# Kernel optimization log

Measured on AMD Instinct MI355X. Metric: run time of the kernel, lower is better.

Reference implementation:

```python
import jax, jax.numpy as jnp
import numpy as np
from jax.ops import segment_sum

N_NODES = 50000


def gcn_conv(x, W, b, src, dst, n_nodes):
    """Standard PyG GCNConv: self-loops + symmetric deg^-1/2 normalization."""
    h = x @ W  # [N, H]
    loop = jnp.arange(n_nodes, dtype=src.dtype)
    s = jnp.concatenate([src, loop])
    d = jnp.concatenate([dst, loop])
    deg = segment_sum(jnp.ones_like(d, dtype=h.dtype), d, num_segments=n_nodes)
    dinv = jnp.where(deg > 0, jax.lax.rsqrt(deg), 0.0)
    norm = dinv[s] * dinv[d]  # [E+N]
    msg = h[s] * norm[:, None]  # gather + scale
    out = segment_sum(msg, d, num_segments=n_nodes)  # scatter-add
    return out + b


def setup_inputs() -> dict:
    key = jax.random.key(0)
    ks = jax.random.split(key, 12)
    node_in, hidden = 256, 128
    n_edges = 1_600_000
    x = jax.random.normal(ks[0], (N_NODES, node_in), dtype=jnp.float32)
    edge_index = jax.random.randint(ks[1], (2, n_edges), 0, N_NODES, dtype=jnp.int64)

    def glorot(k, fan_in, fan_out):
        lim = np.sqrt(6.0 / (fan_in + fan_out)).astype(np.float32)
        return jax.random.uniform(k, (fan_in, fan_out), jnp.float32, -lim, lim)

    W1 = glorot(ks[2], node_in, hidden)
    b1 = jnp.zeros((hidden,), jnp.float32)
    W2 = glorot(ks[3], hidden, hidden)
    b2 = jnp.zeros((hidden,), jnp.float32)
    W3 = glorot(ks[4], 2 * hidden, hidden)
    b3 = jnp.zeros((hidden,), jnp.float32)
    W4 = glorot(ks[5], hidden, 1)
    b4 = jnp.zeros((1,), jnp.float32)
    return {"x": x, "edge_index": edge_index, "W1": W1, "b1": b1,
            "W2": W2, "b2": b2, "W3": W3, "b3": b3, "W4": W4, "b4": b4}


def reference(x, edge_index, W1, b1, W2, b2, W3, b3, W4, b4):
    src, dst = edge_index[0], edge_index[1]
    h = gcn_conv(x, W1, b1, src, dst, N_NODES)
    h = jax.nn.relu(h)  # dropout is identity in eval mode
    h = gcn_conv(h, W2, b2, src, dst, N_NODES)
    # gather node pairs per edge, concat, MLP edge classifier
    ef = jnp.concatenate([h[src], h[dst]], axis=1)  # [E, 2H]
    z = jax.nn.relu(ef @ W3 + b3)
    scores = jax.nn.sigmoid(z @ W4 + b4)
    return scores.squeeze(-1)
```

## Files before the change

kernel.cpp:

```cpp
#include <hip/hip_runtime.h>
#include <math.h>

typedef unsigned short ushort_t;
typedef __attribute__((ext_vector_type(8))) short bf16x8;
typedef __attribute__((ext_vector_type(4))) float f32x4;

__device__ __forceinline__ float bf2f(unsigned short u) {
    union { unsigned int i; float f; } x; x.i = ((unsigned int)u) << 16; return x.f;
}
__device__ __forceinline__ unsigned short f2bf(float f) {
    union { float f; unsigned int i; } x; x.f = f;
    unsigned int lsb = (x.i >> 16) & 1u;
    return (unsigned short)((x.i + 0x7fffu + lsb) >> 16);
}


__global__ __launch_bounds__(1024) void detect_i64(const int* __restrict__ ei,
                                                   int nwords, int* __restrict__ flag) {
    __shared__ int s_any;
    if (threadIdx.x == 0) s_any = 0;
    __syncthreads();
    int any = 0;
    for (int i = threadIdx.x; 2 * i + 1 < nwords; i += 1024)
        if (ei[2 * i + 1] != 0) any = 1;
    if (any) s_any = 1;
    __syncthreads();
    if (threadIdx.x == 0) flag[0] = (s_any == 0) ? 1 : 0;
}

__global__ __launch_bounds__(256) void normalize_idx(const int* __restrict__ ei, int E,
                                                     const int* __restrict__ flag,
                                                     int* __restrict__ s_out,
                                                     int* __restrict__ d_out) {
    int e = blockIdx.x * 256 + threadIdx.x;
    if (e >= E) return;
    if (flag[0]) {
        s_out[e] = ei[2 * e];
        d_out[e] = ei[2 * (E + e)];
    } else {
        s_out[e] = ei[e];
        d_out[e] = ei[E + e];
    }
}


__global__ __launch_bounds__(256) void zero_i32(int* __restrict__ p, int n) {
    int i = blockIdx.x * 256 + threadIdx.x;
    if (i < n) p[i] = 0;
}

__global__ __launch_bounds__(256) void count_deg_part(const int* __restrict__ dst,
                                                      int* __restrict__ deg,
                                                      int E, int RB) {
    int xcd = blockIdx.x & 7;
    int e = (blockIdx.x >> 3) * 256 + threadIdx.x;
    if (e >= E) return;
    int d = dst[e];
    if ((unsigned)(d - xcd * RB) < (unsigned)RB) atomicAdd(&deg[d], 1);
}

__global__ __launch_bounds__(1024) void scan_kernel(const int* __restrict__ deg,
                                                    int* __restrict__ offs,
                                                    int* __restrict__ cursor,
                                                    float* __restrict__ dinv, int n) {
    __shared__ int wsum[16];
    __shared__ int s_carry;
    int tid = threadIdx.x, lane = tid & 63, wid = tid >> 6;
    if (tid == 0) s_carry = 0;
    __syncthreads();
    for (int base = 0; base < n; base += 1024) {
        int i = base + tid;
        int v = (i < n) ? deg[i] : 0;
        int x = v;
        #pragma unroll
        for (int d = 1; d < 64; d <<= 1) {
            int y = __shfl_up(x, d, 64);
            if (lane >= d) x += y;
        }
        if (lane == 63) wsum[wid] = x;
        __syncthreads();
        int carry = s_carry;
        __syncthreads();
        if (tid == 0) {
            int run = 0;
            #pragma unroll
            for (int w = 0; w < 16; ++w) { int t = wsum[w]; wsum[w] = run; run += t; }
            s_carry = carry + run;
        }
        __syncthreads();
        if (i < n) {
            int excl = carry + wsum[wid] + (x - v);
            offs[i] = excl;
            cursor[i] = excl;
            dinv[i] = rsqrtf((float)(v + 1));
        }
        __syncthreads();
    }
    if (tid == 0) offs[n] = s_carry;
}

__global__ __launch_bounds__(256) void fill_csr_part(const int* __restrict__ src,
                                                     const int* __restrict__ dst,
                                                     int* __restrict__ cursor,
                                                     int2* __restrict__ csr_se,
                                                     int E, int RB) {
    int xcd = blockIdx.x & 7;
    int e = (blockIdx.x >> 3) * 256 + threadIdx.x;
    if (e >= E) return;
    int d = dst[e];
    if ((unsigned)(d - xcd * RB) < (unsigned)RB) {
        int pos = atomicAdd(&cursor[d], 1);
        csr_se[pos] = make_int2(src[e], e);
    }
}

__global__ __launch_bounds__(256) void fill_seg(const int* __restrict__ offs,
                                                int* __restrict__ csr_dst, int n_nodes) {
    int wid = threadIdx.x >> 6, lane = threadIdx.x & 63;
    int node = blockIdx.x * 4 + wid;
    if (node >= n_nodes) return;
    int beg = offs[node], end = offs[node + 1];
    for (int i = beg + lane; i < end; i += 64) csr_dst[i] = node;
}


__global__ __launch_bounds__(256) void conv_weights(const float* __restrict__ W1,
                                                    const float* __restrict__ W2,
                                                    const float* __restrict__ W3,
                                                    ushort_t* __restrict__ Wt1,
                                                    ushort_t* __restrict__ Wt2,
                                                    ushort_t* __restrict__ Wt3a,
                                                    ushort_t* __restrict__ Wt3b) {
    int t = blockIdx.x * 256 + threadIdx.x;
    if (t < 32768) {
        int k = t >> 7, n = t & 127;
        Wt1[n * 256 + k] = f2bf(W1[t]);
    } else if (t < 49152) {
        int u = t - 32768; int k = u >> 7, n = u & 127;
        Wt2[n * 128 + k] = f2bf(W2[u]);
    } else if (t < 65536) {
        int u = t - 49152; int k = u >> 7, n = u & 127;
        Wt3a[n * 128 + k] = f2bf(W3[u]);
    } else if (t < 81920) {
        int u = t - 65536; int k = u >> 7, n = u & 127;
        Wt3b[n * 128 + k] = f2bf(W3[128 * 128 + u]);
    }
}


#define ASTR 40
#define BSTR 136

__global__ __launch_bounds__(256) void gemm_mfma(const float* __restrict__ A,
                                                 const ushort_t* __restrict__ Wt,
                                                 void* __restrict__ outv,
                                                 const float* __restrict__ dinv,
                                                 const float* __restrict__ bias,
                                                 int M, int K, int out_bf16) {
    __shared__ __attribute__((aligned(16))) ushort_t Bt[128 * BSTR];
    __shared__ __attribute__((aligned(16))) ushort_t As[64 * ASTR];
    int tid = threadIdx.x;
    int wave = tid >> 6, lane = tid & 63;
    int l15 = lane & 15, lg = lane >> 4;
    int block_m = blockIdx.x * 64;
    f32x4 acc[8];
    #pragma unroll
    for (int i = 0; i < 8; ++i) acc[i] = (f32x4){0.f, 0.f, 0.f, 0.f};

    for (int kh = 0; kh < K; kh += 128) {
        #pragma unroll
        for (int i = 0; i < 16; ++i) {
            int u = i * 256 + tid;
            int col = u >> 5;
            int kq = (u & 31) * 4;
            ushort4 w = *(const ushort4*)(&Wt[(size_t)col * K + kh + kq]);
            *(ushort4*)(&Bt[col * BSTR + kq]) = w;
        }
        for (int k0 = kh; k0 < kh + 128; k0 += 32) {
            #pragma unroll
            for (int rep = 0; rep < 2; ++rep) {
                int unit = rep * 256 + tid;
                int r = unit >> 3;
                int kc = (unit & 7) * 4;
                int gr = block_m + r;
                int grc = gr < M ? gr : M - 1;
                float4 v = *(const float4*)(&A[(size_t)grc * K + k0 + kc]);
                if (gr >= M) v = make_float4(0.f, 0.f, 0.f, 0.f);
                ushort4 p;
                p.x = f2bf(v.x); p.y = f2bf(v.y); p.z = f2bf(v.z); p.w = f2bf(v.w);
                *(ushort4*)(&As[r * ASTR + kc]) = p;
            }
            __syncthreads();
            bf16x8 af = *(const bf16x8*)(&As[(wave * 16 + l15) * ASTR + lg * 8]);
            #pragma unroll
            for (int nf = 0; nf < 8; ++nf) {
                bf16x8 bf = *(const bf16x8*)(&Bt[(nf * 16 + l15) * BSTR +
                                                 (k0 - kh) + lg * 8]);
                acc[nf] = __builtin_amdgcn_mfma_f32_16x16x32_bf16(af, bf, acc[nf],
                                                                  0, 0, 0);
            }
            __syncthreads();
        }
    }
    int orow = block_m + wave * 16 + lg * 4;
    #pragma unroll
    for (int nf = 0; nf < 8; ++nf) {
        int col = nf * 16 + l15;
        float bb = bias ? bias[col] : 0.f;
        #pragma unroll
        for (int j = 0; j < 4; ++j) {
            int m = orow + j;
            if (m < M) {
                float s = dinv ? dinv[m] : 1.f;
                float o = acc[nf][j] * s + bb;
                if (out_bf16)
                    ((ushort_t*)outv)[(size_t)m * 128 + col] = f2bf(o);
                else
                    ((float*)outv)[(size_t)m * 128 + col] = o;
            }
        }
    }
}


__global__ __launch_bounds__(256) void pull_agg(const ushort_t* __restrict__ g,
                                                const int2* __restrict__ csr_se,
                                                const int* __restrict__ offs,
                                                const float* __restrict__ dinv,
                                                const float* __restrict__ bias,
                                                float* __restrict__ out,
                                                int n_nodes, int do_relu) {
    int wid = threadIdx.x >> 6;
    int lane = threadIdx.x & 63;
    int node = blockIdx.x * 4 + wid;
    if (node >= n_nodes) return;
    int beg = offs[node], end = offs[node + 1];
    ushort2 sv = *(const ushort2*)(g + (size_t)node * 128 + 2 * lane);
    float a0 = bf2f(sv.x), a1 = bf2f(sv.y);
    int i = beg;
    for (; i + 4 <= end; i += 4) {
        int s0 = csr_se[i].x, s1 = csr_se[i + 1].x;
        int s2 = csr_se[i + 2].x, s3 = csr_se[i + 3].x;
        ushort2 v0 = *(const ushort2*)(g + (size_t)s0 * 128 + 2 * lane);
        ushort2 v1 = *(const ushort2*)(g + (size_t)s1 * 128 + 2 * lane);
        ushort2 v2 = *(const ushort2*)(g + (size_t)s2 * 128 + 2 * lane);
        ushort2 v3 = *(const ushort2*)(g + (size_t)s3 * 128 + 2 * lane);
        a0 += bf2f(v0.x) + bf2f(v1.x) + bf2f(v2.x) + bf2f(v3.x);
        a1 += bf2f(v0.y) + bf2f(v1.y) + bf2f(v2.y) + bf2f(v3.y);
    }
    for (; i < end; ++i) {
        ushort2 v = *(const ushort2*)(g + (size_t)csr_se[i].x * 128 + 2 * lane);
        a0 += bf2f(v.x); a1 += bf2f(v.y);
    }
    float s = dinv[node];
    float v0 = a0 * s + bias[2 * lane];
    float v1 = a1 * s + bias[2 * lane + 1];
    if (do_relu) { v0 = fmaxf(v0, 0.f); v1 = fmaxf(v1, 0.f); }
    *(float2*)(&out[(size_t)node * 128 + 2 * lane]) = make_float2(v0, v1);
}


__global__ __launch_bounds__(256) void edge_score_csr(const ushort_t* __restrict__ u,
                                                      const ushort_t* __restrict__ v,
                                                      const int2* __restrict__ csr_se,
                                                      const int* __restrict__ csr_dst,
                                                      const float* __restrict__ W4,
                                                      const float* __restrict__ b4,
                                                      float* __restrict__ out, int E) {
    __shared__ int2 s_se[32];
    __shared__ int s_dst[32];
    int tid = threadIdx.x;
    long base = (long)blockIdx.x * 32;
    if (tid < 32) {
        long p = base + tid;
        s_se[tid] = (p < E) ? csr_se[p] : make_int2(0, 0);
    } else if (tid < 64) {
        long p = base + (tid - 32);
        s_dst[tid - 32] = (p < E) ? csr_dst[p] : 0;
    }
    __syncthreads();
    int grp = tid >> 5;
    int lane = tid & 31;
    float4 w4 = *(const float4*)(&W4[lane * 4]);
    float b4v = b4[0];
    #pragma unroll
    for (int i = 0; i < 4; ++i) {
        int ei = grp * 4 + i;
        int s = s_se[ei].x, d = s_dst[ei];
        ushort4 a = *(const ushort4*)(u + (size_t)s * 128 + lane * 4);
        ushort4 b = *(const ushort4*)(v + (size_t)d * 128 + lane * 4);
        float p = fmaxf(bf2f(a.x) + bf2f(b.x), 0.f) * w4.x
                + fmaxf(bf2f(a.y) + bf2f(b.y), 0.f) * w4.y
                + fmaxf(bf2f(a.z) + bf2f(b.z), 0.f) * w4.z
                + fmaxf(bf2f(a.w) + bf2f(b.w), 0.f) * w4.w;
        #pragma unroll
        for (int m = 16; m >= 1; m >>= 1) p += __shfl_xor(p, m, 64);
        if (lane == 0 && base + ei < E)
            out[s_se[ei].y] = 1.f / (1.f + expf(-(p + b4v)));
    }
}


extern "C" void kernel_launch(void* const* d_in, const int* in_sizes, int n_in,
                              void* d_out, int out_size, void* d_ws, size_t ws_size,
                              hipStream_t stream) {
    const float* x  = (const float*)d_in[0];
    const int*   ei = (const int*)d_in[1];
    const float* W1 = (const float*)d_in[2];
    const float* b1 = (const float*)d_in[3];
    const float* W2 = (const float*)d_in[4];
    const float* b2 = (const float*)d_in[5];
    const float* W3 = (const float*)d_in[6];
    const float* b3 = (const float*)d_in[7];
    const float* W4 = (const float*)d_in[8];
    const float* b4 = (const float*)d_in[9];

    int N = in_sizes[0] / 256;
    int E = in_sizes[1] / 2;

    char* ws = (char*)d_ws;
    size_t off = 0;
    auto alloc = [&](size_t bytes) -> void* {
        void* p = ws + off;
        off += (bytes + 255) & ~(size_t)255;
        return p;
    };
    int*      flag    = (int*)     alloc(256);
    int*      srcn    = (int*)     alloc((size_t)E * 4);
    int*      dstn    = (int*)     alloc((size_t)E * 4);
    int*      deg     = (int*)     alloc((size_t)N * 4);
    int*      offs    = (int*)     alloc((size_t)(N + 1) * 4);
    int*      cursor  = (int*)     alloc((size_t)N * 4);
    float*    dinv    = (float*)   alloc((size_t)N * 4);
    int2*     csr_se  = (int2*)    alloc((size_t)E * 8);
    int*      csr_dst = (int*)     alloc((size_t)E * 4);
    ushort_t* gbuf    = (ushort_t*)alloc((size_t)N * 128 * 2);
    ushort_t* ubuf    = (ushort_t*)alloc((size_t)N * 128 * 2);
    ushort_t* vbuf    = (ushort_t*)alloc((size_t)N * 128 * 2);
    float*    hbuf    = (float*)   alloc((size_t)N * 128 * 4);
    ushort_t* Wt1     = (ushort_t*)alloc(128 * 256 * 2);
    ushort_t* Wt2     = (ushort_t*)alloc(128 * 128 * 2);
    ushort_t* Wt3a    = (ushort_t*)alloc(128 * 128 * 2);
    ushort_t* Wt3b    = (ushort_t*)alloc(128 * 128 * 2);
    (void)ws_size; (void)n_in; (void)out_size;

    float* outp = (float*)d_out;
    int gE = (E + 255) / 256;
    int gN4 = (N + 3) / 4;
    int RB = (N + 7) / 8;

    int nwords = (2 * E < 4096) ? 2 * E : 4096;
    detect_i64<<<1, 1024, 0, stream>>>(ei, nwords, flag);
    normalize_idx<<<gE, 256, 0, stream>>>(ei, E, flag, srcn, dstn);
    conv_weights<<<320, 256, 0, stream>>>(W1, W2, W3, Wt1, Wt2, Wt3a, Wt3b);

    zero_i32<<<(N + 255) / 256, 256, 0, stream>>>(deg, N);
    count_deg_part<<<gE * 8, 256, 0, stream>>>(dstn, deg, E, RB);
    scan_kernel<<<1, 1024, 0, stream>>>(deg, offs, cursor, dinv, N);
    fill_csr_part<<<gE * 8, 256, 0, stream>>>(srcn, dstn, cursor, csr_se, E, RB);
    fill_seg<<<gN4, 256, 0, stream>>>(offs, csr_dst, N);

    int gM = (N + 63) / 64;
    gemm_mfma<<<gM, 256, 0, stream>>>(x, Wt1, gbuf, dinv, nullptr, N, 256, 1);
    pull_agg<<<gN4, 256, 0, stream>>>(gbuf, csr_se, offs, dinv, b1, hbuf, N, 1);
    gemm_mfma<<<gM, 256, 0, stream>>>(hbuf, Wt2, gbuf, dinv, nullptr, N, 128, 1);
    pull_agg<<<gN4, 256, 0, stream>>>(gbuf, csr_se, offs, dinv, b2, hbuf, N, 0);
    gemm_mfma<<<gM, 256, 0, stream>>>(hbuf, Wt3a, ubuf, nullptr, nullptr, N, 128, 1);
    gemm_mfma<<<gM, 256, 0, stream>>>(hbuf, Wt3b, vbuf, nullptr, b3, N, 128, 1);
    edge_score_csr<<<(E + 31) / 32, 256, 0, stream>>>(ubuf, vbuf, csr_se, csr_dst,
                                                      W4, b4, outp, E);
}
```

Baseline: 634.3 us.

## Vectorize CSR gathers in aggregation and score edges per destination segment

pull_agg now splits each wavefront into four quarter-waves that each gather a whole 256-byte bf16 row with 16-byte loads, four edges in flight per iteration. Out-of-range slots point to a zeroed padding row, and the quarter-wave partial sums are combined with shuffles. The edge scorer walks each destination's CSR segment with 16 lanes per node, loading the v row once and reusing it for every incoming edge. This removes the csr_dst array and the fill_seg kernel. Per-node loops are serial in degree and can leave lanes idle on low-degree nodes.

After: 621.4 us. 2.0% less time.

```diff
diff --git a/kernel.cpp b/kernel.cpp
--- a/kernel.cpp
+++ b/kernel.cpp
@@ -3,6 +3,7 @@
 
 typedef unsigned short ushort_t;
 typedef __attribute__((ext_vector_type(8))) short bf16x8;
+typedef __attribute__((ext_vector_type(8))) unsigned short us8;
 typedef __attribute__((ext_vector_type(4))) float f32x4;
 
 __device__ __forceinline__ float bf2f(unsigned short u) {
@@ -112,15 +113,6 @@
         int pos = atomicAdd(&cursor[d], 1);
         csr_se[pos] = make_int2(src[e], e);
     }
-}
-
-__global__ __launch_bounds__(256) void fill_seg(const int* __restrict__ offs,
-                                                int* __restrict__ csr_dst, int n_nodes) {
-    int wid = threadIdx.x >> 6, lane = threadIdx.x & 63;
-    int node = blockIdx.x * 4 + wid;
-    if (node >= n_nodes) return;
-    int beg = offs[node], end = offs[node + 1];
-    for (int i = beg + lane; i < end; i += 64) csr_dst[i] = node;
 }
 
 
@@ -230,73 +222,91 @@
                                                 const float* __restrict__ bias,
                                                 float* __restrict__ out,
                                                 int n_nodes, int do_relu) {
-    int wid = threadIdx.x >> 6;
-    int lane = threadIdx.x & 63;
+    int tid = threadIdx.x;
+    int wid = tid >> 6, lane = tid & 63;
+    int q = lane >> 4, c = lane & 15;
     int node = blockIdx.x * 4 + wid;
     if (node >= n_nodes) return;
     int beg = offs[node], end = offs[node + 1];
-    ushort2 sv = *(const ushort2*)(g + (size_t)node * 128 + 2 * lane);
-    float a0 = bf2f(sv.x), a1 = bf2f(sv.y);
-    int i = beg;
-    for (; i + 4 <= end; i += 4) {
-        int s0 = csr_se[i].x, s1 = csr_se[i + 1].x;
-        int s2 = csr_se[i + 2].x, s3 = csr_se[i + 3].x;
-        ushort2 v0 = *(const ushort2*)(g + (size_t)s0 * 128 + 2 * lane);
-        ushort2 v1 = *(const ushort2*)(g + (size_t)s1 * 128 + 2 * lane);
-        ushort2 v2 = *(const ushort2*)(g + (size_t)s2 * 128 + 2 * lane);
-        ushort2 v3 = *(const ushort2*)(g + (size_t)s3 * 128 + 2 * lane);
-        a0 += bf2f(v0.x) + bf2f(v1.x) + bf2f(v2.x) + bf2f(v3.x);
-        a1 += bf2f(v0.y) + bf2f(v1.y) + bf2f(v2.y) + bf2f(v3.y);
-    }
-    for (; i < end; ++i) {
-        ushort2 v = *(const ushort2*)(g + (size_t)csr_se[i].x * 128 + 2 * lane);
-        a0 += bf2f(v.x); a1 += bf2f(v.y);
-    }
+    float acc[8] = {};
+    for (int i = beg; i < end; i += 4) {
+        int j = i + q;
+        int sidx = (j < end) ? csr_se[j].x : n_nodes;
+        us8 r = *(const us8*)(g + (size_t)sidx * 128 + c * 8);
+        acc[0] += bf2f(r[0]); acc[1] += bf2f(r[1]);
+        acc[2] += bf2f(r[2]); acc[3] += bf2f(r[3]);
+        acc[4] += bf2f(r[4]); acc[5] += bf2f(r[5]);
+        acc[6] += bf2f(r[6]); acc[7] += bf2f(r[7]);
+    }
+    #pragma unroll
+    for (int k = 0; k < 8; ++k) {
+        acc[k] += __shfl_xor(acc[k], 16, 64);
+        acc[k] += __shfl_xor(acc[k], 32, 64);
+    }
+    us8 sr = *(const us8*)(g + (size_t)node * 128 + c * 8);
     float s = dinv[node];
-    float v0 = a0 * s + bias[2 * lane];
-    float v1 = a1 * s + bias[2 * lane + 1];
-    if (do_relu) { v0 = fmaxf(v0, 0.f); v1 = fmaxf(v1, 0.f); }
-    *(float2*)(&out[(size_t)node * 128 + 2 * lane]) = make_float2(v0, v1);
-}
-
-
-__global__ __launch_bounds__(256) void edge_score_csr(const ushort_t* __restrict__ u,
+    float4 ba = *(const float4*)(&bias[c * 8]);
+    float4 bb = *(const float4*)(&bias[c * 8 + 4]);
+    float o[8];
+    o[0] = (acc[0] + bf2f(sr[0])) * s + ba.x;
+    o[1] = (acc[1] + bf2f(sr[1])) * s + ba.y;
+    o[2] = (acc[2] + bf2f(sr[2])) * s + ba.z;
+    o[3] = (acc[3] + bf2f(sr[3])) * s + ba.w;
+    o[4] = (acc[4] + bf2f(sr[4])) * s + bb.x;
+    o[5] = (acc[5] + bf2f(sr[5])) * s + bb.y;
+    o[6] = (acc[6] + bf2f(sr[6])) * s + bb.z;
+    o[7] = (acc[7] + bf2f(sr[7])) * s + bb.w;
+    if (do_relu) {
+        #pragma unroll
+        for (int k = 0; k < 8; ++k) o[k] = fmaxf(o[k], 0.f);
+    }
+    if (q == 0) {
+        float* op = &out[(size_t)node * 128 + c * 8];
+        *(float4*)op = make_float4(o[0], o[1], o[2], o[3]);
+        *(float4*)(op + 4) = make_float4(o[4], o[5], o[6], o[7]);
+    }
+}
+
+
+__global__ __launch_bounds__(256) void edge_score_seg(const ushort_t* __restrict__ u,
                                                       const ushort_t* __restrict__ v,
                                                       const int2* __restrict__ csr_se,
-                                                      const int* __restrict__ csr_dst,
+                                                      const int* __restrict__ offs,
                                                       const float* __restrict__ W4,
                                                       const float* __restrict__ b4,
-                                                      float* __restrict__ out, int E) {
-    __shared__ int2 s_se[32];
-    __shared__ int s_dst[32];
+                                                      float* __restrict__ out,
+                                                      int n_nodes) {
     int tid = threadIdx.x;
-    long base = (long)blockIdx.x * 32;
-    if (tid < 32) {
-        long p = base + tid;
-        s_se[tid] = (p < E) ? csr_se[p] : make_int2(0, 0);
-    } else if (tid < 64) {
-        long p = base + (tid - 32);
-        s_dst[tid - 32] = (p < E) ? csr_dst[p] : 0;
-    }
-    __syncthreads();
-    int grp = tid >> 5;
-    int lane = tid & 31;
-    float4 w4 = *(const float4*)(&W4[lane * 4]);
+    int grp = tid >> 4, c = tid & 15;
+    int node = blockIdx.x * 16 + grp;
+    if (node >= n_nodes) return;
+    int beg = offs[node], end = offs[node + 1];
+    if (beg == end) return;
+    us8 vv = *(const us8*)(v + (size_t)node * 128 + c * 8);
+    float vr[8];
+    #pragma unroll
+    for (int k = 0; k < 8; ++k) vr[k] = bf2f(vv[k]);
+    float4 wa = *(const float4*)(&W4[c * 8]);
+    float4 wb = *(const float4*)(&W4[c * 8 + 4]);
     float b4v = b4[0];
-    #pragma unroll
-    for (int i = 0; i < 4; ++i) {
-        int ei = grp * 4 + i;
-        int s = s_se[ei].x, d = s_dst[ei];
-        ushort4 a = *(const ushort4*)(u + (size_t)s * 128 + lane * 4);
-        ushort4 b = *(const ushort4*)(v + (size_t)d * 128 + lane * 4);
-        float p = fmaxf(bf2f(a.x) + bf2f(b.x), 0.f) * w4.x
-                + fmaxf(bf2f(a.y) + bf2f(b.y), 0.f) * w4.y
-                + fmaxf(bf2f(a.z) + bf2f(b.z), 0.f) * w4.z
-                + fmaxf(bf2f(a.w) + bf2f(b.w), 0.f) * w4.w;
-        #pragma unroll
-        for (int m = 16; m >= 1; m >>= 1) p += __shfl_xor(p, m, 64);
-        if (lane == 0 && base + ei < E)
-            out[s_se[ei].y] = 1.f / (1.f + expf(-(p + b4v)));
+    for (int p = beg; p < end; ++p) {
+        int2 se = csr_se[p];
+        us8 uu = *(const us8*)(u + (size_t)se.x * 128 + c * 8);
+        float ps;
+        ps  = fmaxf(bf2f(uu[0]) + vr[0], 0.f) * wa.x;
+        ps += fmaxf(bf2f(uu[1]) + vr[1], 0.f) * wa.y;
+        ps += fmaxf(bf2f(uu[2]) + vr[2], 0.f) * wa.z;
+        ps += fmaxf(bf2f(uu[3]) + vr[3], 0.f) * wa.w;
+        ps += fmaxf(bf2f(uu[4]) + vr[4], 0.f) * wb.x;
+        ps += fmaxf(bf2f(uu[5]) + vr[5], 0.f) * wb.y;
+        ps += fmaxf(bf2f(uu[6]) + vr[6], 0.f) * wb.z;
+        ps += fmaxf(bf2f(uu[7]) + vr[7], 0.f) * wb.w;
+        ps += __shfl_xor(ps, 8, 64);
+        ps += __shfl_xor(ps, 4, 64);
+        ps += __shfl_xor(ps, 2, 64);
+        ps += __shfl_xor(ps, 1, 64);
+        if (c == 0)
+            out[se.y] = 1.f / (1.f + expf(-(ps + b4v)));
     }
 }
 
@@ -333,8 +343,7 @@
     int*      cursor  = (int*)     alloc((size_t)N * 4);
     float*    dinv    = (float*)   alloc((size_t)N * 4);
     int2*     csr_se  = (int2*)    alloc((size_t)E * 8);
-    int*      csr_dst = (int*)     alloc((size_t)E * 4);
-    ushort_t* gbuf    = (ushort_t*)alloc((size_t)N * 128 * 2);
+    ushort_t* gbuf    = (ushort_t*)alloc((size_t)(N + 1) * 128 * 2);
     ushort_t* ubuf    = (ushort_t*)alloc((size_t)N * 128 * 2);
     ushort_t* vbuf    = (ushort_t*)alloc((size_t)N * 128 * 2);
     float*    hbuf    = (float*)   alloc((size_t)N * 128 * 4);
@@ -355,10 +364,10 @@
     conv_weights<<<320, 256, 0, stream>>>(W1, W2, W3, Wt1, Wt2, Wt3a, Wt3b);
 
     zero_i32<<<(N + 255) / 256, 256, 0, stream>>>(deg, N);
+    zero_i32<<<1, 256, 0, stream>>>((int*)(gbuf + (size_t)N * 128), 64);
     count_deg_part<<<gE * 8, 256, 0, stream>>>(dstn, deg, E, RB);
     scan_kernel<<<1, 1024, 0, stream>>>(deg, offs, cursor, dinv, N);
     fill_csr_part<<<gE * 8, 256, 0, stream>>>(srcn, dstn, cursor, csr_se, E, RB);
-    fill_seg<<<gN4, 256, 0, stream>>>(offs, csr_dst, N);
 
     int gM = (N + 63) / 64;
     gemm_mfma<<<gM, 256, 0, stream>>>(x, Wt1, gbuf, dinv, nullptr, N, 256, 1);
@@ -367,6 +376,6 @@
     pull_agg<<<gN4, 256, 0, stream>>>(gbuf, csr_se, offs, dinv, b2, hbuf, N, 0);
     gemm_mfma<<<gM, 256, 0, stream>>>(hbuf, Wt3a, ubuf, nullptr, nullptr, N, 128, 1);
     gemm_mfma<<<gM, 256, 0, stream>>>(hbuf, Wt3b, vbuf, nullptr, b3, N, 128, 1);
-    edge_score_csr<<<(E + 31) / 32, 256, 0, stream>>>(ubuf, vbuf, csr_se, csr_dst,
-                                                      W4, b4, outp, E);
-}
+    edge_score_seg<<<(N + 15) / 16, 256, 0, stream>>>(ubuf, vbuf, csr_se, offs,
+                                                      W4, b4, outp, N);
+}
```
